# Optimization experiments

Measured on AMD Instinct MI355X. Metric: run time of the kernel, lower is better.

## Reference

```python
import jax, jax.numpy as jnp
import numpy as np

NUM_CLASSES = 19
RADIUS = 2  # hardcoded in the original forward
B, H, W = 2, 1024, 2048

# Math note: the original computes, per class k, dist = edt(onehot_pad) + edt(1-onehot_pad)
# (scipy edt = distance to nearest zero). At every pixel exactly one term is nonzero, and it
# equals the Euclidean distance to the nearest opposite-valued pixel WITHIN the zero-padded
# array. Then dist[dist > 2] = 0 and edgemap = (sum_k dist_k) > 0. Hence a pixel is an edge
# pixel iff for some class k its Euclidean-disk(2) neighborhood (inside the padded array;
# out-of-bounds pixels never count) contains BOTH a 1 and a 0 of onehot_k. The disk of radius
# 2 is exactly the 13 integer offsets with dx^2+dy^2 <= 4, so we implement this with one
# small convolution counting ones in the disk (c) and comparing against the number of
# in-bounds disk pixels (nb): edge_k = (c > 0) & (c < nb).

def _disk_kernel():
    r = jnp.arange(-RADIUS, RADIUS + 1)
    d2 = r[:, None] ** 2 + r[None, :] ** 2
    return (d2 <= RADIUS ** 2).astype(jnp.float32)[None, None]  # (1,1,5,5), 13 ones


def setup_inputs() -> dict:
    key = jax.random.key(0)
    gtmasks = jax.random.randint(key, (B, 1, H, W), 0, 20, dtype=jnp.int32)
    return {"gtmasks": gtmasks}


def reference(gtmasks) -> jnp.ndarray:
    b, _, h, w = gtmasks.shape
    lab = gtmasks[:, 0].astype(jnp.int32)  # (B,H,W) integer class labels
    classes = jnp.arange(1, NUM_CLASSES + 1, dtype=jnp.int32)
    # one-hot for classes 1..19, padded with a ring of zeros (np.pad constant 0)
    oh = (lab[:, None, :, :] == classes[None, :, None, None]).astype(jnp.float32)  # (B,K,H,W)
    oh = jnp.pad(oh, ((0, 0), (0, 0), (1, 1), (1, 1)))  # (B,K,H+2,W+2)

    k = _disk_kernel()
    x = oh.reshape(b * NUM_CLASSES, 1, h + 2, w + 2)
    pad = [(RADIUS, RADIUS), (RADIUS, RADIUS)]
    c = jax.lax.conv_general_dilated(x, k, (1, 1), pad)  # ones-count in disk, OOB -> 0
    ones = jnp.ones((1, 1, h + 2, w + 2), jnp.float32)
    nb = jax.lax.conv_general_dilated(ones, k, (1, 1), pad)  # in-bounds disk size

    edge_k = (c > 0) & (c < nb)  # disk contains both a 1 and an in-bounds 0
    edge_k = edge_k.reshape(b, NUM_CLASSES, h + 2, w + 2)[:, :, 1:-1, 1:-1]  # crop pad ring
    edge = jnp.any(edge_k, axis=1, keepdims=True)  # (B,1,H,W)
    return edge.astype(jnp.int32)
```

## Files before the change

kernel.cpp:

```cpp
#include <hip/hip_runtime.h>
#include <stdint.h>

namespace {
constexpr int kH = 1024;
constexpr int kW = 2048;
}

__device__ __forceinline__ uint32_t pk2(int lo, int hi) {
    return (uint32_t)lo | ((uint32_t)hi << 16);
}
__device__ __forceinline__ uint32_t pkmin(uint32_t a, uint32_t b) {
    uint32_t d;
    asm("v_pk_min_i16 %0, %1, %2" : "=v"(d) : "v"(a), "v"(b));
    return d;
}
__device__ __forceinline__ uint32_t pkmax(uint32_t a, uint32_t b) {
    uint32_t d;
    asm("v_pk_max_i16 %0, %1, %2" : "=v"(d) : "v"(a), "v"(b));
    return d;
}

__global__ __launch_bounds__(256) void boundary_edge_kernel(const int* __restrict__ lab,
                                                            int* __restrict__ out) {
    const int x0 = (blockIdx.x * 64 + threadIdx.x) * 4;
    const int y0 = (blockIdx.y * 4 + threadIdx.y) * 4;
    const int bi = blockIdx.z;
    const int* img = lab + (size_t)bi * kH * kW;

    const bool hasL = (x0 > 0);
    const bool hasR = (x0 < kW - 4);

    uint32_t r0a[8], r0b[8];
    uint32_t r1mn01[8], r1mx01[8], r1mn23[8], r1mx23[8];
    uint32_t r2mn01[8], r2mx01[8], r2mn23[8], r2mx23[8];

#pragma unroll
    for (int j = 0; j < 8; ++j) {
        const bool needH1 = (j >= 1) && (j <= 6);
        const bool needH2 = (j >= 2) && (j <= 5);
        const int ry = y0 + j - 2;
        const int ryc = min(max(ry, 0), kH - 1);
        const int* rp = img + (size_t)ryc * kW;
        const int4 v = *reinterpret_cast<const int4*>(rp + x0);

        int m2 = v.x, m1 = v.x, p4 = v.w, p5 = v.w;
        if (needH2) {
            if (hasL) { const int2 L = *reinterpret_cast<const int2*>(rp + x0 - 2); m2 = L.x; m1 = L.y; }
            if (hasR) { const int2 R = *reinterpret_cast<const int2*>(rp + x0 + 4); p4 = R.x; p5 = R.y; }
        } else if (needH1) {
            if (hasL) m1 = rp[x0 - 1];
            if (hasR) p4 = rp[x0 + 4];
        }

        const uint32_t A = pk2(v.x, v.y);
        const uint32_t B = pk2(v.z, v.w);
        r0a[j] = A;
        r0b[j] = B;
        if (needH1) {
            const uint32_t L1 = pk2(m1, v.x);
            const uint32_t M  = pk2(v.y, v.z);
            const uint32_t N  = pk2(v.w, p4);
            r1mn01[j] = pkmin(pkmin(L1, A), M);
            r1mx01[j] = pkmax(pkmax(L1, A), M);
            r1mn23[j] = pkmin(pkmin(M, B), N);
            r1mx23[j] = pkmax(pkmax(M, B), N);
            if (needH2) {
                const uint32_t L2 = pk2(m2, m1);
                const uint32_t P  = pk2(p4, p5);
                r2mn01[j] = pkmin(r1mn01[j], pkmin(L2, B));
                r2mx01[j] = pkmax(r1mx01[j], pkmax(L2, B));
                r2mn23[j] = pkmin(r1mn23[j], pkmin(A, P));
                r2mx23[j] = pkmax(r1mx23[j], pkmax(A, P));
            }
        }
    }

    bool xb[4];
#pragma unroll
    for (int i = 0; i < 4; ++i) {
        const int x = x0 + i;
        xb[i] = (x <= 1) | (x >= kW - 2);
    }

#pragma unroll
    for (int k = 0; k < 4; ++k) {
        const uint32_t mn01 = pkmin(pkmin(r2mn01[k + 2], pkmin(r1mn01[k + 1], r1mn01[k + 3])),
                                    pkmin(r0a[k], r0a[k + 4]));
        const uint32_t mx01 = pkmax(pkmax(r2mx01[k + 2], pkmax(r1mx01[k + 1], r1mx01[k + 3])),
                                    pkmax(r0a[k], r0a[k + 4]));
        const uint32_t mn23 = pkmin(pkmin(r2mn23[k + 2], pkmin(r1mn23[k + 1], r1mn23[k + 3])),
                                    pkmin(r0b[k], r0b[k + 4]));
        const uint32_t mx23 = pkmax(pkmax(r2mx23[k + 2], pkmax(r1mx23[k + 1], r1mx23[k + 3])),
                                    pkmax(r0b[k], r0b[k + 4]));

        const int y = y0 + k;
        const bool yb = (y <= 1) | (y >= kH - 2);

        const uint32_t d01 = mn01 ^ mx01;
        const uint32_t d23 = mn23 ^ mx23;

        int res[4];
        res[0] = ((mx01 & 0xFFFFu) != 0u && (((d01 & 0xFFFFu) != 0u) | yb | xb[0])) ? 1 : 0;
        res[1] = ((mx01 >> 16)     != 0u && (((d01 >> 16)     != 0u) | yb | xb[1])) ? 1 : 0;
        res[2] = ((mx23 & 0xFFFFu) != 0u && (((d23 & 0xFFFFu) != 0u) | yb | xb[2])) ? 1 : 0;
        res[3] = ((mx23 >> 16)     != 0u && (((d23 >> 16)     != 0u) | yb | xb[3])) ? 1 : 0;

        *reinterpret_cast<int4*>(out + ((size_t)(bi * kH + y) * kW + x0)) =
            make_int4(res[0], res[1], res[2], res[3]);
    }
}

extern "C" void kernel_launch(void* const* d_in, const int* in_sizes, int n_in,
                              void* d_out, int out_size, void* d_ws, size_t ws_size,
                              hipStream_t stream) {
    const int* lab = (const int*)d_in[0];
    int* out = (int*)d_out;
    dim3 block(64, 4, 1);
    dim3 grid(kW / (64 * 4), kH / (4 * 4), 2);
    boundary_edge_kernel<<<grid, block, 0, stream>>>(lab, out);
}
```

Measured before the change: 12.77 us.

## Replace horizontal halo loads with wavefront shuffles and use nontemporal stores

Each thread previously issued extra global loads for the left and right halo pixels of every row. Now neighbouring lanes exchange their packed edge values through cross-lane shuffles, and only 16 lanes per wave load the halo at the wavefront edges. The final stores become nontemporal to avoid polluting the cache with output. This adds shuffle instructions and lane-dependent branching in exchange for fewer global load instructions.

New measurement: 10.52 us. -17.6%, faster.

```diff
diff --git a/kernel.cpp b/kernel.cpp
--- a/kernel.cpp
+++ b/kernel.cpp
@@ -4,7 +4,10 @@
 namespace {
 constexpr int kH = 1024;
 constexpr int kW = 2048;
+constexpr int kNBX = kW / 256;
 }
+
+typedef int v4i __attribute__((ext_vector_type(4)));
 
 __device__ __forceinline__ uint32_t pk2(int lo, int hi) {
     return (uint32_t)lo | ((uint32_t)hi << 16);
@@ -19,16 +22,34 @@
     asm("v_pk_max_i16 %0, %1, %2" : "=v"(d) : "v"(a), "v"(b));
     return d;
 }
+__device__ __forceinline__ uint32_t algn(uint32_t hi, uint32_t lo) {
+    return (lo >> 16) | (hi << 16);
+}
 
 __global__ __launch_bounds__(256) void boundary_edge_kernel(const int* __restrict__ lab,
                                                             int* __restrict__ out) {
-    const int x0 = (blockIdx.x * 64 + threadIdx.x) * 4;
+    const int lane = threadIdx.x;
+    const int bx = blockIdx.x;
+    const int x0 = (bx * 64 + lane) * 4;
     const int y0 = (blockIdx.y * 4 + threadIdx.y) * 4;
     const int bi = blockIdx.z;
     const int* img = lab + (size_t)bi * kH * kW;
 
-    const bool hasL = (x0 > 0);
-    const bool hasR = (x0 < kW - 4);
+    const bool hasL = (bx > 0);
+    const bool hasR = (bx < kNBX - 1);
+
+    uint32_t hv = 0;
+    {
+        const int j = lane & 7;
+        const int ry = min(max(y0 + j - 2, 0), kH - 1);
+        const bool doL = (lane < 8) && hasL;
+        const bool doR = (lane >= 8) && (lane < 16) && hasR;
+        if (doL | doR) {
+            const int xh = (lane < 8) ? (bx * 256 - 2) : (bx * 256 + 256);
+            const int2 t = *reinterpret_cast<const int2*>(img + (size_t)ry * kW + xh);
+            hv = pk2(t.x, t.y);
+        }
+    }
 
     uint32_t r0a[8], r0b[8];
     uint32_t r1mn01[8], r1mx01[8], r1mn23[8], r1mx23[8];
@@ -36,41 +57,33 @@
 
 #pragma unroll
     for (int j = 0; j < 8; ++j) {
-        const bool needH1 = (j >= 1) && (j <= 6);
-        const bool needH2 = (j >= 2) && (j <= 5);
-        const int ry = y0 + j - 2;
-        const int ryc = min(max(ry, 0), kH - 1);
-        const int* rp = img + (size_t)ryc * kW;
-        const int4 v = *reinterpret_cast<const int4*>(rp + x0);
-
-        int m2 = v.x, m1 = v.x, p4 = v.w, p5 = v.w;
-        if (needH2) {
-            if (hasL) { const int2 L = *reinterpret_cast<const int2*>(rp + x0 - 2); m2 = L.x; m1 = L.y; }
-            if (hasR) { const int2 R = *reinterpret_cast<const int2*>(rp + x0 + 4); p4 = R.x; p5 = R.y; }
-        } else if (needH1) {
-            if (hasL) m1 = rp[x0 - 1];
-            if (hasR) p4 = rp[x0 + 4];
-        }
-
+        const int ry = min(max(y0 + j - 2, 0), kH - 1);
+        const int4 v = *reinterpret_cast<const int4*>(img + (size_t)ry * kW + x0);
         const uint32_t A = pk2(v.x, v.y);
         const uint32_t B = pk2(v.z, v.w);
         r0a[j] = A;
         r0b[j] = B;
-        if (needH1) {
-            const uint32_t L1 = pk2(m1, v.x);
-            const uint32_t M  = pk2(v.y, v.z);
-            const uint32_t N  = pk2(v.w, p4);
+        if (j >= 1 && j <= 6) {
+            uint32_t Bl = __shfl_up(B, 1);
+            uint32_t Ar = __shfl_down(A, 1);
+            const uint32_t fL = hasL ? __shfl(hv, j)     : pk2(v.x, v.x);
+            const uint32_t fR = hasR ? __shfl(hv, j + 8) : pk2(v.w, v.w);
+            if (lane == 0)  Bl = fL;
+            if (lane == 63) Ar = fR;
+
+            const uint32_t L1 = algn(A, Bl);
+            const uint32_t M  = algn(B, A);
+            const uint32_t N  = algn(Ar, B);
+
             r1mn01[j] = pkmin(pkmin(L1, A), M);
             r1mx01[j] = pkmax(pkmax(L1, A), M);
             r1mn23[j] = pkmin(pkmin(M, B), N);
             r1mx23[j] = pkmax(pkmax(M, B), N);
-            if (needH2) {
-                const uint32_t L2 = pk2(m2, m1);
-                const uint32_t P  = pk2(p4, p5);
-                r2mn01[j] = pkmin(r1mn01[j], pkmin(L2, B));
-                r2mx01[j] = pkmax(r1mx01[j], pkmax(L2, B));
-                r2mn23[j] = pkmin(r1mn23[j], pkmin(A, P));
-                r2mx23[j] = pkmax(r1mx23[j], pkmax(A, P));
+            if (j >= 2 && j <= 5) {
+                r2mn01[j] = pkmin(r1mn01[j], pkmin(Bl, B));
+                r2mx01[j] = pkmax(r1mx01[j], pkmax(Bl, B));
+                r2mn23[j] = pkmin(r1mn23[j], pkmin(A, Ar));
+                r2mx23[j] = pkmax(r1mx23[j], pkmax(A, Ar));
             }
         }
     }
@@ -99,14 +112,14 @@
         const uint32_t d01 = mn01 ^ mx01;
         const uint32_t d23 = mn23 ^ mx23;
 
-        int res[4];
-        res[0] = ((mx01 & 0xFFFFu) != 0u && (((d01 & 0xFFFFu) != 0u) | yb | xb[0])) ? 1 : 0;
-        res[1] = ((mx01 >> 16)     != 0u && (((d01 >> 16)     != 0u) | yb | xb[1])) ? 1 : 0;
-        res[2] = ((mx23 & 0xFFFFu) != 0u && (((d23 & 0xFFFFu) != 0u) | yb | xb[2])) ? 1 : 0;
-        res[3] = ((mx23 >> 16)     != 0u && (((d23 >> 16)     != 0u) | yb | xb[3])) ? 1 : 0;
+        v4i r;
+        r.x = ((mx01 & 0xFFFFu) != 0u && (((d01 & 0xFFFFu) != 0u) | yb | xb[0])) ? 1 : 0;
+        r.y = ((mx01 >> 16)     != 0u && (((d01 >> 16)     != 0u) | yb | xb[1])) ? 1 : 0;
+        r.z = ((mx23 & 0xFFFFu) != 0u && (((d23 & 0xFFFFu) != 0u) | yb | xb[2])) ? 1 : 0;
+        r.w = ((mx23 >> 16)     != 0u && (((d23 >> 16)     != 0u) | yb | xb[3])) ? 1 : 0;
 
-        *reinterpret_cast<int4*>(out + ((size_t)(bi * kH + y) * kW + x0)) =
-            make_int4(res[0], res[1], res[2], res[3]);
+        __builtin_nontemporal_store(r,
+            reinterpret_cast<v4i*>(out + ((size_t)(bi * kH + y) * kW + x0)));
     }
 }
 
@@ -116,6 +129,6 @@
     const int* lab = (const int*)d_in[0];
     int* out = (int*)d_out;
     dim3 block(64, 4, 1);
-    dim3 grid(kW / (64 * 4), kH / (4 * 4), 2);
+    dim3 grid(kW / 256, kH / 16, 2);
     boundary_edge_kernel<<<grid, block, 0, stream>>>(lab, out);
 }
```
